# Kernel optimization log

Measured on AMD Instinct MI355X. Metric: run time of the kernel, lower is better.

The kernel has to match this reference:

```python
import jax, jax.numpy as jnp
import numpy as np

B, N, D, H, DEG = 2, 20000, 256, 8, 8
E = N * DEG
EPS = 1e-3  # keras LayerNormalization default epsilon


def layer_norm(x, gamma, beta):
    mu = jnp.mean(x, axis=-1, keepdims=True)
    var = jnp.mean(jnp.square(x - mu), axis=-1, keepdims=True)
    return (x - mu) * jax.lax.rsqrt(var + EPS) * gamma + beta


def setup_inputs() -> dict:
    key = jax.random.key(0)
    ks = jax.random.split(key, 8)
    x = jax.random.normal(ks[0], (B, N, D), dtype=jnp.float32)
    # edge list sorted by source node; every node has DEG out-edges so
    # segment_sum covers all N segments (matches tf.math.segment_sum semantics)
    src = jnp.repeat(jnp.arange(N, dtype=jnp.int64), DEG)
    dst = jax.random.randint(ks[1], (E,), 0, N, dtype=jnp.int64)
    edges = jnp.stack([src, dst], axis=1)  # [E, 2]
    scale = 0.05
    wq = jax.random.normal(ks[2], (D, D), dtype=jnp.float32) * scale
    wk = jax.random.normal(ks[3], (D, D), dtype=jnp.float32) * scale
    wv = jax.random.normal(ks[4], (D, D), dtype=jnp.float32) * scale
    wo = jax.random.normal(ks[5], (D, D), dtype=jnp.float32) * scale
    zeros = jnp.zeros((D,), dtype=jnp.float32)
    ones = jnp.ones((D,), dtype=jnp.float32)
    return {
        "x": x, "edges": edges,
        "wq": wq, "bq": zeros, "wk": wk, "bk": zeros,
        "wv": wv, "bv": zeros, "wo": wo, "bo": zeros,
        "gamma1": ones, "beta1": zeros, "gamma2": ones, "beta2": zeros,
    }


def reference(x, edges, wq, bq, wk, bk, wv, bv, wo, bo, gamma1, beta1, gamma2, beta2):
    b, n, d = x.shape
    h, dh = H, D // H
    xn = layer_norm(x, gamma1, beta1)                      # [B,N,D]
    # QKV projections, split heads, move node axis to front: [N,B,H,dh]
    def proj(w, bias):
        y = (xn @ w + bias).reshape(b, n, h, dh)
        return jnp.transpose(y, (1, 0, 2, 3))
    q, k, v = proj(wq, bq), proj(wk, bk), proj(wv, bv)
    src, dst = edges[:, 0], edges[:, 1]
    q_part = q[src]                                         # [E,B,H,dh]
    k_part = k[dst]
    v_part = v[dst]
    logits = jnp.sum(q_part * k_part, axis=-1, keepdims=True) / jnp.sqrt(
        jnp.asarray(dh, dtype=x.dtype))                     # [E,B,H,1]
    w = jnp.exp(logits)                                     # unnormalized softmax (as in source)
    num = jax.ops.segment_sum(v_part * w, src, num_segments=n)  # [N,B,H,dh]
    den = jax.ops.segment_sum(w, src, num_segments=n)           # [N,B,H,1]
    attn = num / den
    attn = jnp.transpose(attn, (1, 0, 2, 3)).reshape(b, n, d)   # [B,N,D]
    concat = xn + attn                                      # residual uses normed input (source reassigns `inputs`)
    out = layer_norm(concat, gamma2, beta2)
    out = jax.nn.relu(out @ wo + bo)
    return out + concat
```

## Files before the change

### kernel.cpp

```cpp
#include <hip/hip_runtime.h>


typedef __bf16 bf16x8 __attribute__((ext_vector_type(8)));
typedef float  f32x4  __attribute__((ext_vector_type(4)));

__device__ __forceinline__ float bf2f(unsigned short u) {
    union { unsigned int i; float f; } v; v.i = ((unsigned int)u) << 16; return v.f;
}
__device__ __forceinline__ unsigned short f2bf(float f) {
    union { float f; unsigned int i; } v; v.f = f;
    unsigned int x = v.i;
    unsigned int r = (x + 0x7FFFu + ((x >> 16) & 1u)) >> 16;
    return (unsigned short)r;
}

#define NNODE 20000
#define ROWS  40000
#define DMODEL 256

__global__ __launch_bounds__(256) void prep_ln1_kernel(
    const float* __restrict__ wq, const float* __restrict__ wk,
    const float* __restrict__ wv, const float* __restrict__ wo,
    const float* __restrict__ bq, const float* __restrict__ bk,
    const float* __restrict__ bv, const float* __restrict__ bo,
    const float* __restrict__ x,
    const float* __restrict__ g1, const float* __restrict__ b1,
    unsigned short* __restrict__ Wqkvt,
    unsigned short* __restrict__ Wot,
    float* __restrict__ biasq,
    float* __restrict__ biaso,
    unsigned short* __restrict__ xn)
{
    if (blockIdx.x < 1024) {
        int idx = blockIdx.x * 256 + threadIdx.x;
        if (idx < 768 * 256) {
            int n = idx >> 8, k = idx & 255;
            int sel = n >> 8, nl = n & 255;
            const float* w = (sel == 0) ? wq : (sel == 1) ? wk : wv;
            Wqkvt[idx] = f2bf(w[k * 256 + nl]);
        } else {
            int idx2 = idx - 768 * 256;
            int n = idx2 >> 8, k = idx2 & 255;
            Wot[idx2] = f2bf(wo[k * 256 + n]);
        }
        if (idx < 768) {
            const float* bb = (idx < 256) ? bq : (idx < 512) ? bk : bv;
            biasq[idx] = bb[idx & 255];
        }
        if (idx >= 768 && idx < 1024) biaso[idx - 768] = bo[idx - 768];
        return;
    }
    int wave = threadIdx.x >> 6, lane = threadIdx.x & 63;
    int sub = lane >> 5, hl = lane & 31;
    int m = (blockIdx.x - 1024) * 8 + wave * 2 + sub;
    const float* xp = x + (size_t)m * DMODEL + hl * 8;
    float4 x0 = *(const float4*)xp;
    float4 x1 = *(const float4*)(xp + 4);
    float f[8] = {x0.x, x0.y, x0.z, x0.w, x1.x, x1.y, x1.z, x1.w};
    float s = 0.f, ss = 0.f;
    #pragma unroll
    for (int t = 0; t < 8; ++t) { s += f[t]; ss += f[t]*f[t]; }
    #pragma unroll
    for (int mk = 1; mk < 32; mk <<= 1) { s += __shfl_xor(s, mk); ss += __shfl_xor(ss, mk); }
    float mu  = s * (1.f/256.f);
    float var = ss * (1.f/256.f) - mu*mu;
    float rs  = rsqrtf(var + 1e-3f);
    float4 g0 = *(const float4*)(g1 + hl * 8);
    float4 g1v = *(const float4*)(g1 + hl * 8 + 4);
    float4 b0 = *(const float4*)(b1 + hl * 8);
    float4 b1v = *(const float4*)(b1 + hl * 8 + 4);
    float gg[8] = {g0.x, g0.y, g0.z, g0.w, g1v.x, g1v.y, g1v.z, g1v.w};
    float bb[8] = {b0.x, b0.y, b0.z, b0.w, b1v.x, b1v.y, b1v.z, b1v.w};
    unsigned short o[8];
    #pragma unroll
    for (int t = 0; t < 8; ++t) o[t] = f2bf((f[t] - mu) * rs * gg[t] + bb[t]);
    *(int4*)(xn + (size_t)m * DMODEL + hl * 8) = *(const int4*)o;
}

#define BUFSZ (128 * 64)
#define SWZI(r, c) (((r) << 6) + ((c) ^ (((r) & 7) << 3)))
#define MFMA_BF16(d, a, b) d = __builtin_amdgcn_mfma_f32_16x16x32_bf16(a, b, d, 0, 0, 0)
#define LIGHT_BARRIER() do {                                  \
        __builtin_amdgcn_sched_barrier(0);                    \
        asm volatile("s_waitcnt lgkmcnt(0)" ::: "memory");    \
        __builtin_amdgcn_sched_barrier(0);                    \
        __builtin_amdgcn_s_barrier();                         \
        __builtin_amdgcn_sched_barrier(0);                    \
    } while (0)

template<bool EPI>
__global__ __launch_bounds__(1024, 8) void gemm_kernel(
    const unsigned short* __restrict__ A,
    const unsigned short* __restrict__ Bt,
    const float* __restrict__ bias,
    void* __restrict__ C,
    const unsigned short* __restrict__ resid,
    int M, int Ncols)
{
    __shared__ __align__(16) unsigned short As[2 * BUFSZ];
    __shared__ __align__(16) unsigned short Bs[2 * BUFSZ];
    int tid  = threadIdx.x;
    int wave = tid >> 6, lane = tid & 63;
    int quad = lane >> 4, l16 = lane & 15;

    int nt_total = Ncols >> 7;
    int nwg = gridDim.x;
    int xcd = blockIdx.x & 7, loc = blockIdx.x >> 3;
    int qq = nwg >> 3, rr = nwg & 7;
    int wid = (xcd < rr) ? (xcd * (qq + 1) + loc)
                         : (rr * (qq + 1) + (xcd - rr) * qq + loc);
    int mt = wid / nt_total;
    int nt = wid - mt * nt_total;
    int m0 = mt * 128, n0 = nt * 128;
    int wm = (wave >> 2) * 32, wn = (wave & 3) * 32;

    int srow = tid >> 3;
    int scol = (tid & 7) * 8;
    int arow = m0 + srow; if (arow >= M) arow = M - 1;
    const unsigned short* Ap = A  + (size_t)arow * 256 + scol;
    const unsigned short* Bp = Bt + (size_t)(n0 + srow) * 256 + scol;
    int wi0 = SWZI(srow, scol);

    f32x4 acc00 = {}, acc01 = {}, acc10 = {}, acc11 = {};

    int4 s0a, s0b;
    int4 s1a, s1b;

#define STAGE_LOAD(S, KT) do {                         \
        S##a = *(const int4*)(Ap + (KT) * 64);         \
        S##b = *(const int4*)(Bp + (KT) * 64);         \
    } while (0)
#define STAGE_WRITE(S, BUF) do {                       \
        *(int4*)&As[(BUF) * BUFSZ + wi0] = S##a;       \
        *(int4*)&Bs[(BUF) * BUFSZ + wi0] = S##b;       \
    } while (0)
#define COMPUTE(BUF) do {                                                          \
        _Pragma("unroll")                                                          \
        for (int ks = 0; ks < 64; ks += 32) {                                      \
            int ca = ks + quad * 8;                                                \
            int bb = (BUF) * BUFSZ;                                                \
            bf16x8 a0 = *(const bf16x8*)&As[bb + SWZI(wm +  0 + l16, ca)];         \
            bf16x8 a1 = *(const bf16x8*)&As[bb + SWZI(wm + 16 + l16, ca)];         \
            bf16x8 b0 = *(const bf16x8*)&Bs[bb + SWZI(wn +  0 + l16, ca)];         \
            bf16x8 b1 = *(const bf16x8*)&Bs[bb + SWZI(wn + 16 + l16, ca)];         \
            MFMA_BF16(acc00, a0, b0); MFMA_BF16(acc01, a0, b1);                    \
            MFMA_BF16(acc10, a1, b0); MFMA_BF16(acc11, a1, b1);                    \
        }                                                                          \
    } while (0)

    STAGE_LOAD(s0, 0);
    STAGE_LOAD(s1, 1);
    STAGE_WRITE(s0, 0);
    LIGHT_BARRIER();

    STAGE_LOAD(s0, 2);
    COMPUTE(0);
    STAGE_WRITE(s1, 1);
    LIGHT_BARRIER();

    STAGE_LOAD(s1, 3);
    COMPUTE(1);
    STAGE_WRITE(s0, 0);
    LIGHT_BARRIER();

    COMPUTE(0);
    STAGE_WRITE(s1, 1);
    LIGHT_BARRIER();

    COMPUTE(1);

#undef STAGE_LOAD
#undef STAGE_WRITE
#undef COMPUTE

#define EPI_STORE(accv, R, CC) do {                                          \
        int col = n0 + wn + (CC) * 16 + l16;                                 \
        float bb = bias[col];                                                \
        int rowb = m0 + wm + (R) * 16 + quad * 4;                            \
        _Pragma("unroll")                                                    \
        for (int rr = 0; rr < 4; ++rr) {                                     \
            int row = rowb + rr;                                             \
            if (row < M) {                                                   \
                float v = (accv)[rr] + bb;                                   \
                if (EPI) {                                                   \
                    v = fmaxf(v, 0.f);                                       \
                    v += bf2f(resid[(size_t)row * 256 + col]);               \
                    ((float*)C)[(size_t)row * Ncols + col] = v;              \
                } else {                                                     \
                    ((unsigned short*)C)[(size_t)row * Ncols + col] = f2bf(v);\
                }                                                            \
            }                                                                \
        }                                                                    \
    } while (0)

    EPI_STORE(acc00, 0, 0); EPI_STORE(acc01, 0, 1);
    EPI_STORE(acc10, 1, 0); EPI_STORE(acc11, 1, 1);
#undef EPI_STORE
}

__global__ __launch_bounds__(1024) void attn_kernel(
    const unsigned short* __restrict__ qkv,
    const int* __restrict__ edges,
    const unsigned short* __restrict__ xn,
    const float* __restrict__ g2, const float* __restrict__ b2,
    unsigned short* __restrict__ concat,
    unsigned short* __restrict__ h2)
{
    int wave = threadIdx.x >> 6, lane = threadIdx.x & 63;
    int i = blockIdx.x * 16 + wave;
    int b = lane >> 5, hl = lane & 31;
    size_t m = (size_t)b * NNODE + i;

    int jv = 0;
    if (lane < 8) jv = edges[2 * (i * 8 + lane) + 1];

    int4 qi = *(const int4*)(qkv + m * 768 + hl * 8);
    int4 xi = *(const int4*)(xn + m * DMODEL + hl * 8);
    const unsigned short* qs = (const unsigned short*)&qi;
    float qf[8];
    #pragma unroll
    for (int t = 0; t < 8; ++t) qf[t] = bf2f(qs[t]);

#define KVLOAD(E)                                                                  \
    int j##E = __shfl(jv, E);                                                      \
    const unsigned short* kp##E = qkv + ((size_t)b * NNODE + j##E) * 768 + 256 + hl * 8; \
    int4 KI##E = *(const int4*)(kp##E);                                            \
    int4 VI##E = *(const int4*)(kp##E + 256);
    KVLOAD(0) KVLOAD(1) KVLOAD(2) KVLOAD(3)
    KVLOAD(4) KVLOAD(5) KVLOAD(6) KVLOAD(7)
#undef KVLOAD

    float acc[8] = {};
    float den = 0.f;
    const float scale = 0.17677669529663687f;
#define EDGE(E) do {                                                         \
        const unsigned short* ks = (const unsigned short*)&KI##E;            \
        const unsigned short* vs = (const unsigned short*)&VI##E;            \
        float dot = 0.f;                                                     \
        _Pragma("unroll")                                                    \
        for (int t = 0; t < 8; ++t) dot += qf[t] * bf2f(ks[t]);              \
        dot += __shfl_xor(dot, 1);                                           \
        dot += __shfl_xor(dot, 2);               \
        float w = __expf(dot * scale);                                       \
        _Pragma("unroll")                                                    \
        for (int t = 0; t < 8; ++t) acc[t] += w * bf2f(vs[t]);               \
        den += w;                                                            \
    } while (0)
    EDGE(0); EDGE(1); EDGE(2); EDGE(3);
    EDGE(4); EDGE(5); EDGE(6); EDGE(7);
#undef EDGE
    float inv = 1.f / den;

    const unsigned short* xs = (const unsigned short*)&xi;
    float c[8], s = 0.f, ss = 0.f;
    #pragma unroll
    for (int t = 0; t < 8; ++t) { c[t] = bf2f(xs[t]) + acc[t] * inv; s += c[t]; ss += c[t]*c[t]; }
    #pragma unroll
    for (int mk = 1; mk < 32; mk <<= 1) { s += __shfl_xor(s, mk); ss += __shfl_xor(ss, mk); }
    float mu  = s * (1.f/256.f);
    float var = ss * (1.f/256.f) - mu*mu;
    float rs  = rsqrtf(var + 1e-3f);

    float4 ga = *(const float4*)(g2 + hl * 8);
    float4 gb = *(const float4*)(g2 + hl * 8 + 4);
    float4 ba = *(const float4*)(b2 + hl * 8);
    float4 bb = *(const float4*)(b2 + hl * 8 + 4);
    float gg[8] = {ga.x, ga.y, ga.z, ga.w, gb.x, gb.y, gb.z, gb.w};
    float bv[8] = {ba.x, ba.y, ba.z, ba.w, bb.x, bb.y, bb.z, bb.w};
    unsigned short oc[8], oh[8];
    #pragma unroll
    for (int t = 0; t < 8; ++t) {
        oc[t] = f2bf(c[t]);
        oh[t] = f2bf((c[t] - mu) * rs * gg[t] + bv[t]);
    }
    *(int4*)(concat + m * DMODEL + hl * 8) = *(const int4*)oc;
    *(int4*)(h2     + m * DMODEL + hl * 8) = *(const int4*)oh;
}

extern "C" void kernel_launch(void* const* d_in, const int* in_sizes, int n_in,
                              void* d_out, int out_size, void* d_ws, size_t ws_size,
                              hipStream_t stream)
{
    const float* x   = (const float*)d_in[0];
    const int* edges = (const int*)d_in[1];
    const float* wq = (const float*)d_in[2];
    const float* bq = (const float*)d_in[3];
    const float* wk = (const float*)d_in[4];
    const float* bk = (const float*)d_in[5];
    const float* wv = (const float*)d_in[6];
    const float* bv = (const float*)d_in[7];
    const float* wo = (const float*)d_in[8];
    const float* bo = (const float*)d_in[9];
    const float* g1 = (const float*)d_in[10];
    const float* b1 = (const float*)d_in[11];
    const float* g2 = (const float*)d_in[12];
    const float* b2 = (const float*)d_in[13];

    char* ws = (char*)d_ws;
    unsigned short* Wqkvt = (unsigned short*)(ws);
    unsigned short* Wot   = (unsigned short*)(ws + 393216);
    float* biasq          = (float*)(ws + 393216 + 131072);
    float* biaso          = (float*)(ws + 393216 + 131072 + 3072);
    size_t off = 393216 + 131072 + 4096;
    unsigned short* xn     = (unsigned short*)(ws + off); off += (size_t)ROWS * DMODEL * 2;
    unsigned short* qkv    = (unsigned short*)(ws + off); off += (size_t)ROWS * 768 * 2;
    unsigned short* concat = (unsigned short*)(ws + off); off += (size_t)ROWS * DMODEL * 2;
    unsigned short* h2     = (unsigned short*)(ws + off); off += (size_t)ROWS * DMODEL * 2;

    prep_ln1_kernel<<<1024 + ROWS / 8, 256, 0, stream>>>(
        wq, wk, wv, wo, bq, bk, bv, bo, x, g1, b1, Wqkvt, Wot, biasq, biaso, xn);
    gemm_kernel<false><<<dim3(313 * 6), 1024, 0, stream>>>(xn, Wqkvt, biasq, qkv, nullptr, ROWS, 768);
    attn_kernel<<<NNODE / 16, 1024, 0, stream>>>(qkv, edges, xn, g2, b2, concat, h2);
    gemm_kernel<true><<<dim3(313 * 2), 1024, 0, stream>>>(h2, Wot, biaso, d_out, concat, ROWS, 256);
}
```

Baseline: 218.3 us.

## Tile weight transpose through LDS and reorder GEMM stage writes before compute

The weight conversion and transpose now runs as 64 blocks that each load a 64x64 tile with coalesced float4 reads, transpose it through padded LDS, and write bf16 rows with 16-byte stores. The biases move to a separate block, which replaces 1024 blocks of strided scalar gathers. In the GEMM, each LDS stage write is issued before the MFMA compute on the other buffer rather than after it, and the compute is wrapped in s_setprio raise and lower calls. The aim is to cut prep-kernel time and overlap LDS writes with matrix math, at the cost of higher LDS and register pressure in the GEMM.

Result: faster. 213.2 us (-2.4%).

```diff
diff --git a/kernel.cpp b/kernel.cpp
--- a/kernel.cpp
+++ b/kernel.cpp
@@ -31,28 +31,61 @@
     float* __restrict__ biaso,
     unsigned short* __restrict__ xn)
 {
-    if (blockIdx.x < 1024) {
-        int idx = blockIdx.x * 256 + threadIdx.x;
-        if (idx < 768 * 256) {
-            int n = idx >> 8, k = idx & 255;
-            int sel = n >> 8, nl = n & 255;
-            const float* w = (sel == 0) ? wq : (sel == 1) ? wk : wv;
-            Wqkvt[idx] = f2bf(w[k * 256 + nl]);
+    if (blockIdx.x < 64) {
+        __shared__ unsigned short lds[64 * 72];
+        int t = blockIdx.x;
+        const float* w;
+        unsigned short* outp;
+        int k0, n0, orow_base;
+        if (t < 48) {
+            int sel = t >> 4, tt = t & 15;
+            w = (sel == 0) ? wq : (sel == 1) ? wk : wv;
+            k0 = (tt & 3) * 64; n0 = (tt >> 2) * 64;
+            outp = Wqkvt; orow_base = sel * 256 + n0;
         } else {
-            int idx2 = idx - 768 * 256;
-            int n = idx2 >> 8, k = idx2 & 255;
-            Wot[idx2] = f2bf(wo[k * 256 + n]);
+            int tt = t - 48;
+            w = wo;
+            k0 = (tt & 3) * 64; n0 = (tt >> 2) * 64;
+            outp = Wot; orow_base = n0;
         }
-        if (idx < 768) {
-            const float* bb = (idx < 256) ? bq : (idx < 512) ? bk : bv;
-            biasq[idx] = bb[idx & 255];
+        int tid = threadIdx.x;
+        int r = tid >> 2, cseg = (tid & 3) * 16;
+        const float* wp = w + (size_t)(k0 + r) * 256 + n0 + cseg;
+        float4 v0 = *(const float4*)(wp);
+        float4 v1 = *(const float4*)(wp + 4);
+        float4 v2 = *(const float4*)(wp + 8);
+        float4 v3 = *(const float4*)(wp + 12);
+        float vv[16] = {v0.x,v0.y,v0.z,v0.w, v1.x,v1.y,v1.z,v1.w,
+                        v2.x,v2.y,v2.z,v2.w, v3.x,v3.y,v3.z,v3.w};
+        #pragma unroll
+        for (int j = 0; j < 16; ++j) lds[r * 72 + cseg + j] = f2bf(vv[j]);
+        __syncthreads();
+        int orow = tid >> 2, oseg = (tid & 3) * 16;
+        __align__(16) unsigned short o[16];
+        #pragma unroll
+        for (int j = 0; j < 16; ++j) o[j] = lds[(oseg + j) * 72 + orow];
+        unsigned short* op = outp + (size_t)(orow_base + orow) * 256 + k0 + oseg;
+        *(int4*)(op)     = ((const int4*)o)[0];
+        *(int4*)(op + 8) = ((const int4*)o)[1];
+        return;
+    }
+    if (blockIdx.x == 64) {
+        int tid = threadIdx.x;
+        #pragma unroll
+        for (int rr = 0; rr < 4; ++rr) {
+            int idx = rr * 256 + tid;
+            if (idx < 768) {
+                const float* bb = (idx < 256) ? bq : (idx < 512) ? bk : bv;
+                biasq[idx] = bb[idx & 255];
+            } else {
+                biaso[idx - 768] = bo[idx - 768];
+            }
         }
-        if (idx >= 768 && idx < 1024) biaso[idx - 768] = bo[idx - 768];
         return;
     }
     int wave = threadIdx.x >> 6, lane = threadIdx.x & 63;
     int sub = lane >> 5, hl = lane & 31;
-    int m = (blockIdx.x - 1024) * 8 + wave * 2 + sub;
+    int m = (blockIdx.x - 65) * 8 + wave * 2 + sub;
     const float* xp = x + (size_t)m * DMODEL + hl * 8;
     float4 x0 = *(const float4*)xp;
     float4 x1 = *(const float4*)(xp + 4);
@@ -135,6 +168,7 @@
         *(int4*)&Bs[(BUF) * BUFSZ + wi0] = S##b;       \
     } while (0)
 #define COMPUTE(BUF) do {                                                          \
+        __builtin_amdgcn_s_setprio(1);                                             \
         _Pragma("unroll")                                                          \
         for (int ks = 0; ks < 64; ks += 32) {                                      \
             int ca = ks + quad * 8;                                                \
@@ -146,6 +180,7 @@
             MFMA_BF16(acc00, a0, b0); MFMA_BF16(acc01, a0, b1);                    \
             MFMA_BF16(acc10, a1, b0); MFMA_BF16(acc11, a1, b1);                    \
         }                                                                          \
+        __builtin_amdgcn_s_setprio(0);                                             \
     } while (0)
 
     STAGE_LOAD(s0, 0);
@@ -154,17 +189,17 @@
     LIGHT_BARRIER();
 
     STAGE_LOAD(s0, 2);
+    STAGE_WRITE(s1, 1);
     COMPUTE(0);
+    LIGHT_BARRIER();
+
+    STAGE_LOAD(s1, 3);
+    STAGE_WRITE(s0, 0);
+    COMPUTE(1);
+    LIGHT_BARRIER();
+
     STAGE_WRITE(s1, 1);
-    LIGHT_BARRIER();
-
-    STAGE_LOAD(s1, 3);
-    COMPUTE(1);
-    STAGE_WRITE(s0, 0);
-    LIGHT_BARRIER();
-
     COMPUTE(0);
-    STAGE_WRITE(s1, 1);
     LIGHT_BARRIER();
 
     COMPUTE(1);
@@ -307,7 +342,7 @@
     unsigned short* concat = (unsigned short*)(ws + off); off += (size_t)ROWS * DMODEL * 2;
     unsigned short* h2     = (unsigned short*)(ws + off); off += (size_t)ROWS * DMODEL * 2;
 
-    prep_ln1_kernel<<<1024 + ROWS / 8, 256, 0, stream>>>(
+    prep_ln1_kernel<<<65 + ROWS / 8, 256, 0, stream>>>(
         wq, wk, wv, wo, bq, bk, bv, bo, x, g1, b1, Wqkvt, Wot, biasq, biaso, xn);
     gemm_kernel<false><<<dim3(313 * 6), 1024, 0, stream>>>(xn, Wqkvt, biasq, qkv, nullptr, ROWS, 768);
     attn_kernel<<<NNODE / 16, 1024, 0, stream>>>(qkv, edges, xn, g2, b2, concat, h2);
```
